# Kernel tuning notes

Measured on AMD Instinct MI355X. Metric: run time of the kernel, lower is better.

## Reference

```python
import jax, jax.numpy as jnp
import numpy as np

TOPK = 80
RADIUS_GAIN = 14.0
RADIUS_MIN = 1.5
RADIUS_MAX = 18.0
EPS = 1e-6


def _norm01(x, eps=EPS):
    # per-batch min/max normalization over all non-batch dims
    b = x.shape[0]
    flat = x.reshape(b, -1)
    mn = flat.min(axis=1).reshape(b, 1, 1, 1)
    mx = flat.max(axis=1).reshape(b, 1, 1, 1)
    return (x - mn) / (mx - mn + eps)


def _avg_pool(x, k):
    # torch avg_pool2d(kernel=k, stride=1, padding=k//2, count_include_pad=True)
    s = jax.lax.reduce_window(x, 0.0, jax.lax.add, (1, 1, k, k), (1, 1, 1, 1), 'SAME')
    return s / float(k * k)


def _max_pool(x, k):
    return jax.lax.reduce_window(x, -jnp.inf, jax.lax.max, (1, 1, k, k), (1, 1, 1, 1), 'SAME')


def _compact_connected_prior(score_map):
    occ = (score_map > 0.2).astype(score_map.dtype)
    local_occ = _avg_pool(occ, 9)
    local_mass = _avg_pool(score_map, 9)
    compact = _norm01(local_occ * local_mass)
    return score_map * compact


def _gaussian_map(score_map, depth):
    b, _, h, w = score_map.shape
    dtype = score_map.dtype
    pooled = _max_pool(score_map, 5)
    maxima = score_map * (score_map == pooled).astype(dtype)  # NMS keep local maxima

    flat = maxima.reshape(b, h * w)
    vals, inds = jax.lax.top_k(flat, TOPK)              # [B,K]
    vals = jnp.where(vals > 0, vals, jnp.zeros_like(vals))  # zero-weight masked peaks

    ys = (inds // w).astype(dtype)                       # [B,K]
    xs = (inds % w).astype(dtype)
    z = jnp.take_along_axis(depth.reshape(b, h * w), inds, axis=1)
    z = jnp.maximum(z, 1e-3)
    radius = jnp.clip(RADIUS_GAIN / z, RADIUS_MIN, RADIUS_MAX)
    sigma2 = (0.6 * radius) ** 2                         # [B,K]

    yy = jnp.arange(h, dtype=dtype)
    xx = jnp.arange(w, dtype=dtype)
    dx2 = (xx[None, None, None, :] - xs[:, :, None, None]) ** 2   # [B,K,1,W]
    dy2 = (yy[None, None, :, None] - ys[:, :, None, None]) ** 2   # [B,K,H,1]
    maps = vals[:, :, None, None] * jnp.exp(
        -(dx2 + dy2) / (2.0 * sigma2[:, :, None, None] + 1e-6))    # [B,K,H,W]
    gauss = maps.max(axis=1)[:, None]                    # [B,1,H,W]; maps>=0 so zero baseline preserved
    return _norm01(gauss)


def setup_inputs() -> dict:
    key = jax.random.key(0)
    k1, k2 = jax.random.split(key)
    B, H, W = 8, 320, 320
    voxel_score_map = jax.random.uniform(k1, (B, 1, H, W), dtype=jnp.float32)
    # depth within the module's valid z range [0.3, 20.0]
    depth = 0.3 + 19.7 * jax.random.uniform(k2, (B, 1, H, W), dtype=jnp.float32)
    return {'voxel_score_map': voxel_score_map, 'depth': depth}


def reference(voxel_score_map, depth):
    compact_score = _compact_connected_prior(voxel_score_map)
    return _gaussian_map(compact_score, depth)
```

## Files before the change

### kernel.cpp

```cpp
#include <hip/hip_runtime.h>
#include <math.h>

#define HH 320
#define WW 320
#define HWP (HH * WW)
#define KTOP 80
#define CNT_STRIDE 64
#define CAP (HWP / 2)
#define TS 16
#define TPR (WW / TS)
#define TPI (TPR * (HH / TS))
#define TW 32
#define TH 64
#define NTPRX (WW / TW)
#define NTPI (NTPRX * (HH / TH))
#define LOG2E 1.4426950408889634f
#define NLOG2TAU 19.931568569324174f

__device__ __forceinline__ void wave_minmax(float& mn, float& mx) {
    for (int off = 32; off > 0; off >>= 1) {
        mn = fminf(mn, __shfl_xor(mn, off, 64));
        mx = fmaxf(mx, __shfl_xor(mx, off, 64));
    }
}

__global__ __launch_bounds__(256) void pool_fused_k(
        const float* __restrict__ score, float* __restrict__ prod,
        float2* __restrict__ pmm, int* __restrict__ cand_cnt, int B_) {
    int tid = threadIdx.x;
    if (blockIdx.x == 0)
        for (int t = tid; t < B_ * CNT_STRIDE; t += 256) cand_cnt[t] = 0;
    int blk = blockIdx.x;
    int b = blk / NTPI, t = blk % NTPI;
    int ty0 = (t / NTPRX) * TH, tx0 = (t % NTPRX) * TW;
    __shared__ float rss[TH + 8][TW + 4];
    __shared__ float rso[TH + 8][TW + 4];
    const float4* img4 = (const float4*)(score + b * HWP);
    for (int i = tid; i < (TH + 8) * (TW / 4); i += 256) {
        int r = i / (TW / 4), q = i % (TW / 4);
        int gy = ty0 - 4 + r;
        float o0=0,o1=0,o2=0,o3=0,p0=0,p1=0,p2=0,p3=0;
        if (gy >= 0 && gy < HH) {
            const float4* row4 = img4 + gy * (WW / 4);
            int gq = tx0 / 4 + q;
            float4 a = (gq > 0) ? row4[gq - 1] : make_float4(0,0,0,0);
            float4 bb = row4[gq];
            float4 c = (gq < WW / 4 - 1) ? row4[gq + 1] : make_float4(0,0,0,0);
            float w0=a.x,w1=a.y,w2=a.z,w3=a.w,w4=bb.x,w5=bb.y,w6=bb.z,w7=bb.w,w8=c.x,w9=c.y,w10=c.z,w11=c.w;
            float s = w0+w1+w2+w3+w4+w5+w6+w7+w8;
            o0=s; s+=w9-w0; o1=s; s+=w10-w1; o2=s; s+=w11-w2; o3=s;
            float c0=(w0>0.2f)?1.f:0.f, c1=(w1>0.2f)?1.f:0.f, c2=(w2>0.2f)?1.f:0.f, c3=(w3>0.2f)?1.f:0.f;
            float c4=(w4>0.2f)?1.f:0.f, c5=(w5>0.2f)?1.f:0.f, c6=(w6>0.2f)?1.f:0.f, c7=(w7>0.2f)?1.f:0.f;
            float c8=(w8>0.2f)?1.f:0.f, c9=(w9>0.2f)?1.f:0.f, c10=(w10>0.2f)?1.f:0.f, c11=(w11>0.2f)?1.f:0.f;
            float u = c0+c1+c2+c3+c4+c5+c6+c7+c8;
            p0=u; u+=c9-c0; p1=u; u+=c10-c1; p2=u; u+=c11-c2; p3=u;
        }
        *(float4*)&rss[r][q * 4] = make_float4(o0,o1,o2,o3);
        *(float4*)&rso[r][q * 4] = make_float4(p0,p1,p2,p3);
    }
    __syncthreads();
    float tmn = INFINITY, tmx = 0.f;
    const float inv81 = 1.0f / 81.0f;
    float4* pr4 = (float4*)(prod + b * HWP);
    for (int i = tid; i < TH * (TW / 4); i += 256) {
        int r = i / (TW / 4), q = i % (TW / 4);
        float sx=0,sy=0,sz=0,sw=0, ox=0,oy=0,oz=0,ow=0;
#pragma unroll
        for (int j = 0; j < 9; ++j) {
            float4 s = *(float4*)&rss[r + j][q * 4];
            float4 o = *(float4*)&rso[r + j][q * 4];
            sx+=s.x; sy+=s.y; sz+=s.z; sw+=s.w;
            ox+=o.x; oy+=o.y; oz+=o.z; ow+=o.w;
        }
        float px=(ox*inv81)*(sx*inv81), py=(oy*inv81)*(sy*inv81);
        float pz=(oz*inv81)*(sz*inv81), pw=(ow*inv81)*(sw*inv81);
        pr4[(ty0 + r) * (WW / 4) + tx0 / 4 + q] = make_float4(px,py,pz,pw);
        tmn = fminf(tmn, fminf(fminf(px,py), fminf(pz,pw)));
        tmx = fmaxf(tmx, fmaxf(fmaxf(px,py), fmaxf(pz,pw)));
    }
    wave_minmax(tmn, tmx);
    __shared__ float wmn[4], wmx[4];
    int w = tid >> 6;
    if ((tid & 63) == 0) { wmn[w] = tmn; wmx[w] = tmx; }
    __syncthreads();
    if (tid == 0)
        pmm[blk] = make_float2(fminf(fminf(wmn[0],wmn[1]), fminf(wmn[2],wmn[3])),
                               fmaxf(fmaxf(wmx[0],wmx[1]), fmaxf(wmx[2],wmx[3])));
}

__global__ __launch_bounds__(256) void cs_nms_k(
        const float* __restrict__ score, const float* __restrict__ prod,
        const float2* __restrict__ pmm, float* __restrict__ cand_base,
        int* __restrict__ cand_cnt) {
    int tid = threadIdx.x;
    int blk = blockIdx.x;
    int b = blk / NTPI, t = blk % NTPI;
    int ty0 = (t / NTPRX) * TH, tx0 = (t % NTPRX) * TW;
    float tmn = INFINITY, tmx = 0.f;
    if (tid < NTPI) { float2 e = pmm[b * NTPI + tid]; tmn = e.x; tmx = e.y; }
    wave_minmax(tmn, tmx);
    __shared__ float s_mn, s_inv;
    if (tid == 0) { s_mn = tmn; s_inv = 1.0f / (tmx - tmn + 1e-6f); }
    __shared__ float cs[TH + 4][TW + 8 + 4];
    __shared__ float rm[TH + 4][TW + 4];
    __syncthreads();
    float mn = s_mn, inv = s_inv;
    const float4* sc4 = (const float4*)(score + b * HWP);
    const float4* pr4 = (const float4*)(prod + b * HWP);
    for (int i = tid; i < (TH + 4) * 10; i += 256) {
        int r = i / 10, q = i % 10;
        int gy = ty0 - 2 + r;
        int gq = tx0 / 4 - 1 + q;
        float4 c4 = make_float4(0,0,0,0);
        if (gy >= 0 && gy < HH && gq >= 0 && gq < WW / 4) {
            float4 s4 = sc4[gy * (WW / 4) + gq];
            float4 p4 = pr4[gy * (WW / 4) + gq];
            c4.x = s4.x * ((p4.x - mn) * inv); c4.y = s4.y * ((p4.y - mn) * inv);
            c4.z = s4.z * ((p4.z - mn) * inv); c4.w = s4.w * ((p4.w - mn) * inv);
        }
        *(float4*)&cs[r][q * 4] = c4;
    }
    __syncthreads();
    for (int i = tid; i < (TH + 4) * (TW / 4); i += 256) {
        int r = i / (TW / 4), x = (i % (TW / 4)) * 4;
        float c0=cs[r][x+2], c1=cs[r][x+3], c2=cs[r][x+4], c3=cs[r][x+5];
        float c4v=cs[r][x+6], c5=cs[r][x+7], c6=cs[r][x+8], c7=cs[r][x+9];
        float m01=fmaxf(c0,c1), m23=fmaxf(c2,c3), m45=fmaxf(c4v,c5), m67=fmaxf(c6,c7);
        float r0 = fmaxf(fmaxf(m01, m23), c4v);
        float r1 = fmaxf(fmaxf(c1, m23), m45);
        float r2 = fmaxf(fmaxf(m23, m45), c6);
        float r3 = fmaxf(fmaxf(c3, m45), m67);
        *(float4*)&rm[r][x] = make_float4(r0,r1,r2,r3);
    }
    __syncthreads();
    bool cd[8]; float vv[8]; int pb[2]; int offs[8];
#pragma unroll
    for (int qq = 0; qq < 2; ++qq) {
        int quad = qq * 256 + tid;
        int r = quad >> 3, x = (quad & 7) * 4;
        float4 v = *(float4*)&cs[r + 2][x + 4];
        float4 nm = *(float4*)&rm[r][x];
#pragma unroll
        for (int k = 1; k <= 4; ++k) {
            float4 rr = *(float4*)&rm[r + k][x];
            nm.x=fmaxf(nm.x,rr.x); nm.y=fmaxf(nm.y,rr.y);
            nm.z=fmaxf(nm.z,rr.z); nm.w=fmaxf(nm.w,rr.w);
        }
        pb[qq] = (ty0 + r) * WW + tx0 + x;
        cd[qq*4+0] = v.x > 0.f && v.x >= nm.x; vv[qq*4+0] = v.x;
        cd[qq*4+1] = v.y > 0.f && v.y >= nm.y; vv[qq*4+1] = v.y;
        cd[qq*4+2] = v.z > 0.f && v.z >= nm.z; vv[qq*4+2] = v.z;
        cd[qq*4+3] = v.w > 0.f && v.w >= nm.w; vv[qq*4+3] = v.w;
    }
    int lane = tid & 63, w = tid >> 6;
    unsigned long long lower = (1ULL << lane) - 1ULL;
    int wave_run = 0;
#pragma unroll
    for (int j = 0; j < 8; ++j) {
        unsigned long long m = __ballot(cd[j]);
        offs[j] = wave_run + __popcll(m & lower);
        wave_run += __popcll(m);
    }
    __shared__ int wbase[4];
    __shared__ int blockbase;
    if (lane == 0) wbase[w] = wave_run;
    __syncthreads();
    if (tid == 0) {
        int a0=wbase[0], a1=wbase[1], a2=wbase[2], a3=wbase[3];
        int tot = a0+a1+a2+a3;
        wbase[0]=0; wbase[1]=a0; wbase[2]=a0+a1; wbase[3]=a0+a1+a2;
        blockbase = tot ? atomicAdd(&cand_cnt[b * CNT_STRIDE], tot) : 0;
    }
    __syncthreads();
    float* cv = cand_base + b * HWP;
    int* ci = (int*)(cand_base + b * HWP + CAP);
    int bb2 = blockbase + wbase[w];
#pragma unroll
    for (int j = 0; j < 8; ++j) {
        if (cd[j]) {
            int slot = bb2 + offs[j];
            if (slot < CAP) { cv[slot] = vv[j]; ci[slot] = pb[j >> 2] + (j & 3); }
        }
    }
}

__global__ __launch_bounds__(1024) void topk_k(
        const float* __restrict__ cand_base, const int* __restrict__ cand_cnt,
        const float* __restrict__ depth, float4* __restrict__ pk4g) {
    int b = blockIdx.x;
    int tid = threadIdx.x;
    int n = cand_cnt[b * CNT_STRIDE];
    if (n > CAP) n = CAP;
    const float* cv = cand_base + b * HWP;
    const int* ci = (const int*)(cand_base + b * HWP + CAP);

    __shared__ int hist[256];
    __shared__ unsigned s_prefix;
    __shared__ int s_kth;
    __shared__ float sel_v[KTOP];
    __shared__ int sel_i[KTOP];
    __shared__ int s_ng, s_nt;
    __shared__ int tie_i[512];
    __shared__ float s_lvoff;

    if (tid == 0) { s_prefix = 0; s_kth = KTOP; s_ng = 0; s_nt = 0; }
    if (tid < KTOP) { sel_v[tid] = 0.f; sel_i[tid] = -1; }
    __syncthreads();

    if (n > KTOP) {
        for (int shift = 24; shift >= 0; shift -= 8) {
            if (tid < 256) hist[tid] = 0;
            __syncthreads();
            unsigned pref = s_prefix;
            unsigned hmask = (shift == 24) ? 0u : (0xFFFFFFFFu << (shift + 8));
            for (int i = tid; i < n; i += 1024) {
                unsigned u = __float_as_uint(cv[i]);
                if ((u & hmask) == (pref & hmask))
                    atomicAdd(&hist[(u >> shift) & 255], 1);
            }
            __syncthreads();
            if (tid < 64) {
                int h0 = hist[tid*4+0], h1 = hist[tid*4+1], h2 = hist[tid*4+2], h3 = hist[tid*4+3];
                int ls3 = h3, ls2 = h2 + ls3, ls1 = h1 + ls2, ls0 = h0 + ls1;
                int sum = ls0;
                for (int off = 1; off < 64; off <<= 1) {
                    int vv2 = __shfl_down(sum, off, 64);
                    if (tid + off < 64) sum += vv2;
                }
                int excl = sum - ls0;
                int kth = s_kth;
                int SS0=ls0+excl, SS1=ls1+excl, SS2=ls2+excl, SS3=ls3+excl, SS4=excl;
                unsigned pr = s_prefix;
                int bin = -1, rem = 0;
                if (SS0 >= kth && SS1 < kth) { bin = tid*4+0; rem = kth - SS1; }
                else if (SS1 >= kth && SS2 < kth) { bin = tid*4+1; rem = kth - SS2; }
                else if (SS2 >= kth && SS3 < kth) { bin = tid*4+2; rem = kth - SS3; }
                else if (SS3 >= kth && SS4 < kth) { bin = tid*4+3; rem = kth - SS4; }
                if (bin >= 0) { s_prefix = pr | ((unsigned)bin << shift); s_kth = rem; }
            }
            __syncthreads();
        }
        unsigned T = s_prefix;
        int need_eq = s_kth;
        for (int i = tid; i < n; i += 1024) {
            unsigned u = __float_as_uint(cv[i]);
            if (u > T) {
                int s2 = atomicAdd(&s_ng, 1);
                if (s2 < KTOP) { sel_v[s2] = cv[i]; sel_i[s2] = ci[i]; }
            } else if (u == T) {
                int s2 = atomicAdd(&s_nt, 1);
                if (s2 < 512) tie_i[s2] = ci[i];
            }
        }
        __syncthreads();
        int G = s_ng; if (G > KTOP) G = KTOP;
        int nt = s_nt; if (nt > 512) nt = 512;
        for (int t2 = tid; t2 < nt; t2 += 1024) {
            int mine = tie_i[t2];
            int rank = 0;
            for (int j = 0; j < nt; ++j)
                if (tie_i[j] < mine) rank++;
            if (rank < need_eq && G + rank < KTOP) {
                sel_v[G + rank] = __uint_as_float(T);
                sel_i[G + rank] = mine;
            }
        }
        __syncthreads();
    } else {
        for (int i = tid; i < n; i += 1024) { sel_v[i] = cv[i]; sel_i[i] = ci[i]; }
        __syncthreads();
    }

    if (tid < 64) {
        float vmv = sel_v[tid];
        if (tid + 64 < KTOP) vmv = fmaxf(vmv, sel_v[tid + 64]);
        for (int off = 32; off > 0; off >>= 1) vmv = fmaxf(vmv, __shfl_xor(vmv, off, 64));
        if (tid == 0) s_lvoff = log2f(vmv + 1e-6f);
    }
    __syncthreads();

    if (tid < KTOP) {
        float val = sel_v[tid];
        int idx = sel_i[tid];
        float xk = 0.f, yk = 0.f, wv = -1.f, lv = -INFINITY;
        if (val > 0.f && idx >= 0) {
            yk = (float)(idx / WW);
            xk = (float)(idx % WW);
            float z = fmaxf(depth[b * HWP + idx], 1e-3f);
            float r = fminf(fmaxf(14.0f / z, 1.5f), 18.0f);
            float s2 = 0.6f * r;
            s2 = s2 * s2;
            wv = -LOG2E / (2.0f * s2 + 1e-6f);
            lv = log2f(val) - s_lvoff;
        }
        pk4g[b * KTOP + tid] = make_float4(lv, xk, yk, wv);
    }
}

__global__ __launch_bounds__(256) void gauss_out_k(const float4* __restrict__ pk4g,
                                                   float* __restrict__ out) {
    int tb = blockIdx.x, tid = threadIdx.x;
    int b = tb / TPI, t = tb % TPI;
    int ty = t / TPR, tx = t % TPR;
    __shared__ float4 spk[KTOP];
    __shared__ int s_c0, s_cnt;
    bool keep = false;
    float4 pk;
    if (tid < KTOP) {
        pk = pk4g[b * KTOP + tid];
        float cut = (pk.x + NLOG2TAU) / (-pk.w);
        float x0 = (float)(tx * TS), x1 = x0 + (TS - 1);
        float y0 = (float)(ty * TS), y1 = y0 + (TS - 1);
        float cx = fminf(fmaxf(pk.y, x0), x1);
        float cy = fminf(fmaxf(pk.z, y0), y1);
        float dx = pk.y - cx, dy = pk.z - cy;
        keep = (dx * dx + dy * dy) <= cut;
    }
    int lane = tid & 63, w = tid >> 6;
    unsigned long long m = __ballot(keep);
    if (w == 0 && lane == 0) s_c0 = __popcll(m);
    __syncthreads();
    int base = (w == 0) ? 0 : s_c0;
    if (keep) spk[base + __popcll(m & ((1ULL << lane) - 1ULL))] = pk;
    if (w == 1 && lane == 0) s_cnt = s_c0 + __popcll(m);
    __syncthreads();
    int cnt = s_cnt;
    int ly = tid / TS, lx = tid % TS;
    int y = ty * TS + ly, x = tx * TS + lx;
    float fx = (float)x, fy = (float)y;
    float mval = 0.f;
    for (int i = 0; i < cnt; ++i) {
        float4 p = spk[i];
        float dx = fx - p.y, dy = fy - p.z;
        mval = fmaxf(mval, __builtin_amdgcn_exp2f(fmaf(fmaf(dx, dx, dy * dy), p.w, p.x)));
    }
    out[b * HWP + y * WW + x] = mval;
}

extern "C" void kernel_launch(void* const* d_in, const int* in_sizes, int n_in,
                              void* d_out, int out_size, void* d_ws, size_t ws_size,
                              hipStream_t stream) {
    const float* score = (const float*)d_in[0];
    const float* depth = (const float*)d_in[1];
    float* out = (float*)d_out;
    int total = in_sizes[0];
    int B_ = total / HWP;

    float* buf1 = (float*)d_ws;
    float* buf2 = buf1 + total;
    char* small = (char*)(buf2 + total);
    float4* pk4 = (float4*)small;
    int* cand_cnt = (int*)(small + B_ * KTOP * sizeof(float4));
    float2* pmm = (float2*)(cand_cnt + B_ * CNT_STRIDE);

    pool_fused_k<<<B_ * NTPI, 256, 0, stream>>>(score, buf1, pmm, cand_cnt, B_);
    cs_nms_k<<<B_ * NTPI, 256, 0, stream>>>(score, buf1, pmm, buf2, cand_cnt);
    topk_k<<<B_, 1024, 0, stream>>>(buf2, cand_cnt, depth, pk4);
    gauss_out_k<<<B_ * TPI, 256, 0, stream>>>(pk4, out);
}
```

Before: 32.69 us.

## Stage top-k candidates in LDS and widen gaussian tiles to four pixels per thread

When the per-batch candidate count fits in 8192 entries, the top-k kernel copies candidate values into shared memory once with vectorized loads, so the four radix-histogram passes and the selection pass read LDS instead of global memory. The gaussian output kernel now uses 64x16 tiles with four adjacent pixels per thread. This shares the dy term and peak loads across the four pixels and writes the results with float4 stores. In exchange, the larger tiles pass more peaks through the culling test, and the 32KB LDS buffer adds shared-memory pressure to the top-k kernel.

Result: no change. 32.27 us, median of 3 (-1.3%).

```diff
diff --git a/kernel.cpp b/kernel.cpp
--- a/kernel.cpp
+++ b/kernel.cpp
@@ -7,13 +7,15 @@
 #define KTOP 80
 #define CNT_STRIDE 64
 #define CAP (HWP / 2)
-#define TS 16
-#define TPR (WW / TS)
-#define TPI (TPR * (HH / TS))
+#define LVCAP 8192
 #define TW 32
 #define TH 64
 #define NTPRX (WW / TW)
 #define NTPI (NTPRX * (HH / TH))
+#define GSW 64
+#define GSH 16
+#define SPRX (WW / GSW)
+#define SPI (SPRX * (HH / GSH))
 #define LOG2E 1.4426950408889634f
 #define NLOG2TAU 19.931568569324174f
 
@@ -194,6 +196,7 @@
     const float* cv = cand_base + b * HWP;
     const int* ci = (const int*)(cand_base + b * HWP + CAP);
 
+    __shared__ float cvl[LVCAP];
     __shared__ int hist[256];
     __shared__ unsigned s_prefix;
     __shared__ int s_kth;
@@ -203,6 +206,16 @@
     __shared__ int tie_i[512];
     __shared__ float s_lvoff;
 
+    bool inl = (n <= LVCAP);
+    if (inl) {
+        int n4 = n >> 2;
+        const float4* cv4 = (const float4*)cv;
+        for (int i = tid; i < n4; i += 1024) {
+            float4 v = cv4[i];
+            cvl[i*4+0] = v.x; cvl[i*4+1] = v.y; cvl[i*4+2] = v.z; cvl[i*4+3] = v.w;
+        }
+        for (int i = n4 * 4 + tid; i < n; i += 1024) cvl[i] = cv[i];
+    }
     if (tid == 0) { s_prefix = 0; s_kth = KTOP; s_ng = 0; s_nt = 0; }
     if (tid < KTOP) { sel_v[tid] = 0.f; sel_i[tid] = -1; }
     __syncthreads();
@@ -214,7 +227,7 @@
             unsigned pref = s_prefix;
             unsigned hmask = (shift == 24) ? 0u : (0xFFFFFFFFu << (shift + 8));
             for (int i = tid; i < n; i += 1024) {
-                unsigned u = __float_as_uint(cv[i]);
+                unsigned u = __float_as_uint(inl ? cvl[i] : cv[i]);
                 if ((u & hmask) == (pref & hmask))
                     atomicAdd(&hist[(u >> shift) & 255], 1);
             }
@@ -243,10 +256,10 @@
         unsigned T = s_prefix;
         int need_eq = s_kth;
         for (int i = tid; i < n; i += 1024) {
-            unsigned u = __float_as_uint(cv[i]);
+            unsigned u = __float_as_uint(inl ? cvl[i] : cv[i]);
             if (u > T) {
                 int s2 = atomicAdd(&s_ng, 1);
-                if (s2 < KTOP) { sel_v[s2] = cv[i]; sel_i[s2] = ci[i]; }
+                if (s2 < KTOP) { sel_v[s2] = __uint_as_float(u); sel_i[s2] = ci[i]; }
             } else if (u == T) {
                 int s2 = atomicAdd(&s_nt, 1);
                 if (s2 < 512) tie_i[s2] = ci[i];
@@ -299,9 +312,10 @@
 
 __global__ __launch_bounds__(256) void gauss_out_k(const float4* __restrict__ pk4g,
                                                    float* __restrict__ out) {
-    int tb = blockIdx.x, tid = threadIdx.x;
-    int b = tb / TPI, t = tb % TPI;
-    int ty = t / TPR, tx = t % TPR;
+    int blk = blockIdx.x, tid = threadIdx.x;
+    int b = blk / SPI, s = blk % SPI;
+    int sy = s / SPRX, sx = s % SPRX;
+    int y0 = sy * GSH, x0 = sx * GSW;
     __shared__ float4 spk[KTOP];
     __shared__ int s_c0, s_cnt;
     bool keep = false;
@@ -309,10 +323,10 @@
     if (tid < KTOP) {
         pk = pk4g[b * KTOP + tid];
         float cut = (pk.x + NLOG2TAU) / (-pk.w);
-        float x0 = (float)(tx * TS), x1 = x0 + (TS - 1);
-        float y0 = (float)(ty * TS), y1 = y0 + (TS - 1);
-        float cx = fminf(fmaxf(pk.y, x0), x1);
-        float cy = fminf(fmaxf(pk.z, y0), y1);
+        float rx0 = (float)x0, rx1 = (float)(x0 + GSW - 1);
+        float ry0 = (float)y0, ry1 = (float)(y0 + GSH - 1);
+        float cx = fminf(fmaxf(pk.y, rx0), rx1);
+        float cy = fminf(fmaxf(pk.z, ry0), ry1);
         float dx = pk.y - cx, dy = pk.z - cy;
         keep = (dx * dx + dy * dy) <= cut;
     }
@@ -325,16 +339,22 @@
     if (w == 1 && lane == 0) s_cnt = s_c0 + __popcll(m);
     __syncthreads();
     int cnt = s_cnt;
-    int ly = tid / TS, lx = tid % TS;
-    int y = ty * TS + ly, x = tx * TS + lx;
+    int r = tid >> 4, qx = tid & 15;
+    int y = y0 + r, x = x0 + qx * 4;
     float fx = (float)x, fy = (float)y;
-    float mval = 0.f;
+    float m0 = 0.f, m1 = 0.f, m2 = 0.f, m3 = 0.f;
     for (int i = 0; i < cnt; ++i) {
         float4 p = spk[i];
-        float dx = fx - p.y, dy = fy - p.z;
-        mval = fmaxf(mval, __builtin_amdgcn_exp2f(fmaf(fmaf(dx, dx, dy * dy), p.w, p.x)));
-    }
-    out[b * HWP + y * WW + x] = mval;
+        float dy = fy - p.z;
+        float dy2 = dy * dy;
+        float dx0 = fx - p.y;
+        float dx1 = dx0 + 1.f, dx2 = dx0 + 2.f, dx3 = dx0 + 3.f;
+        m0 = fmaxf(m0, __builtin_amdgcn_exp2f(fmaf(fmaf(dx0, dx0, dy2), p.w, p.x)));
+        m1 = fmaxf(m1, __builtin_amdgcn_exp2f(fmaf(fmaf(dx1, dx1, dy2), p.w, p.x)));
+        m2 = fmaxf(m2, __builtin_amdgcn_exp2f(fmaf(fmaf(dx2, dx2, dy2), p.w, p.x)));
+        m3 = fmaxf(m3, __builtin_amdgcn_exp2f(fmaf(fmaf(dx3, dx3, dy2), p.w, p.x)));
+    }
+    *(float4*)&out[b * HWP + y * WW + x] = make_float4(m0, m1, m2, m3);
 }
 
 extern "C" void kernel_launch(void* const* d_in, const int* in_sizes, int n_in,
@@ -356,5 +376,5 @@
     pool_fused_k<<<B_ * NTPI, 256, 0, stream>>>(score, buf1, pmm, cand_cnt, B_);
     cs_nms_k<<<B_ * NTPI, 256, 0, stream>>>(score, buf1, pmm, buf2, cand_cnt);
     topk_k<<<B_, 1024, 0, stream>>>(buf2, cand_cnt, depth, pk4);
-    gauss_out_k<<<B_ * TPI, 256, 0, stream>>>(pk4, out);
-}
+    gauss_out_k<<<B_ * SPI, 256, 0, stream>>>(pk4, out);
+}
```
